# Performance work log

Hardware: AMD Instinct MI355X
Metric: run time of the kernel (lower is better)

Reference implementation:

```python
import jax, jax.numpy as jnp
import numpy as np

N_NODES = 10000
N_EDGES = 320000
D = 128  # feature dim for edges, nodes, globals


def setup_inputs() -> dict:
    key = jax.random.key(0)
    ks = jax.random.split(key, 8)
    edges = jax.random.normal(ks[0], (N_EDGES, D), dtype=jnp.float32)
    nodes = jax.random.normal(ks[1], (N_NODES, D), dtype=jnp.float32)
    globals_ = jax.random.normal(ks[2], (D,), dtype=jnp.float32)
    receivers = jax.random.randint(ks[3], (N_EDGES,), 0, N_NODES, dtype=jnp.int32).astype(jnp.int64)
    senders = jax.random.randint(ks[4], (N_EDGES,), 0, N_NODES, dtype=jnp.int32).astype(jnp.int64)
    W1 = jax.random.normal(ks[5], (4 * D, 256), dtype=jnp.float32) * (1.0 / np.sqrt(4 * D))
    b1 = jnp.zeros((256,), dtype=jnp.float32)
    W2 = jax.random.normal(ks[6], (256, D), dtype=jnp.float32) * (1.0 / np.sqrt(256))
    b2 = jnp.zeros((D,), dtype=jnp.float32)
    return {"edges": edges, "nodes": nodes, "globals_": globals_,
            "receivers": receivers, "senders": senders,
            "W1": W1, "b1": b1, "W2": W2, "b2": b2}


def reference(edges, nodes, globals_, receivers, senders, W1, b1, W2, b2):
    # Gather adjacent node features to edges, broadcast globals, concat.
    recv_feats = nodes[receivers]                 # [E, D]
    send_feats = nodes[senders]                   # [E, D]
    glob_feats = jnp.broadcast_to(globals_, (edges.shape[0], globals_.shape[0]))  # [E, D]
    x = jnp.concatenate([edges, recv_feats, send_feats, glob_feats], axis=-1)     # [E, 4D]
    # Edge-update MLP: 4D -> 256 -> D with relu.
    h = jax.nn.relu(x @ W1 + b1)
    new_edges = h @ W2 + b2                       # [E, D]
    return new_edges
```

## Files before the change

### kernel.cpp

```cpp
#include <hip/hip_runtime.h>
#include <hip/hip_bf16.h>

#define D 128
#define NH 256
#define K1 384
#define BM 64
#define E_TOTAL 320000
#define NNODES 10000

typedef __attribute__((ext_vector_type(8))) short bf16x8;
typedef __attribute__((ext_vector_type(4))) float f32x4;

__device__ __forceinline__ unsigned short f2b(float f) {
  unsigned int u = __builtin_bit_cast(unsigned int, f);
  u += 0x7fffu + ((u >> 16) & 1u);
  return (unsigned short)(u >> 16);
}

__global__ void cast_nodes_kernel(const float* __restrict__ nodes,
                                  ushort* __restrict__ out) {
  int i = (blockIdx.x * 256 + threadIdx.x) * 4;
  float4 v = *(const float4*)(nodes + i);
  ushort4 b;
  b.x = f2b(v.x); b.y = f2b(v.y); b.z = f2b(v.z); b.w = f2b(v.w);
  *(ushort4*)(out + i) = b;
}

__global__ void pack_w1_kernel(const float* __restrict__ W1,
                               ushort* __restrict__ W1p) {
  int c = blockIdx.x * 256 + threadIdx.x;
  int nt = c / (12 * 64);
  int rem = c % (12 * 64);
  int ks = rem >> 6;
  int l = rem & 63;
  int col = nt * 16 + (l & 15);
  int k0 = ks * 32 + (l >> 4) * 8;
  ushort* dst = W1p + (size_t)c * 8;
  #pragma unroll
  for (int j = 0; j < 8; ++j)
    dst[j] = f2b(W1[(size_t)(k0 + j) * NH + col]);
}

__global__ void pack_w2_kernel(const float* __restrict__ W2,
                               ushort* __restrict__ W2p) {
  int c = blockIdx.x * 256 + threadIdx.x;
  int nt2 = c / (8 * 64);
  int rem = c % (8 * 64);
  int ks = rem >> 6;
  int l = rem & 63;
  int col = nt2 * 16 + (l & 15);
  int k0 = ks * 32 + (l >> 4) * 8;
  ushort* dst = W2p + (size_t)c * 8;
  #pragma unroll
  for (int j = 0; j < 8; ++j)
    dst[j] = f2b(W2[(size_t)(k0 + j) * D + col]);
}

__global__ void cvec_kernel(const float* __restrict__ W1,
                            const float* __restrict__ b1,
                            const float* __restrict__ g,
                            float* __restrict__ cvec) {
  int n = threadIdx.x;
  float acc = b1[n];
  for (int k = 0; k < D; ++k)
    acc += g[k] * W1[(size_t)(K1 + k) * NH + n];
  cvec[n] = acc;
}

__global__ __launch_bounds__(512, 4) void fused_kernel(
    const float* __restrict__ edges,
    const ushort* __restrict__ nodes_b,
    const int* __restrict__ receivers,
    const int* __restrict__ senders,
    const ushort* __restrict__ W1p,
    const float* __restrict__ cvec,
    const ushort* __restrict__ W2p,
    const float* __restrict__ b2,
    float* __restrict__ out) {
  __shared__ char Xs[BM * 768];
  __shared__ char Hs[BM * 512];

  const int ebase = blockIdx.x * BM;
  const int tid = threadIdx.x;

  const int gr0 = tid >> 4;
  const int gr1 = gr0 + 32;
  const int gc = (tid & 15) << 3;
  int idx_r0 = receivers[ebase + gr0];
  int idx_r1 = receivers[ebase + gr1];
  int idx_s0 = senders[ebase + gr0];
  int idx_s1 = senders[ebase + gr1];

  float4 ev[4];
  int er[4], ec[4];
  #pragma unroll
  for (int it = 0; it < 4; ++it) {
    int ch = tid + it * 512;
    er[it] = ch >> 5;
    ec[it] = (ch & 31) << 2;
    ev[it] = *(const float4*)(edges + (size_t)(ebase + er[it]) * D + ec[it]);
  }

  uint4 gv[4];
  gv[0] = *(const uint4*)(nodes_b + (size_t)idx_r0 * D + gc);
  gv[1] = *(const uint4*)(nodes_b + (size_t)idx_r1 * D + gc);
  gv[2] = *(const uint4*)(nodes_b + (size_t)idx_s0 * D + gc);
  gv[3] = *(const uint4*)(nodes_b + (size_t)idx_s1 * D + gc);

  #pragma unroll
  for (int it = 0; it < 4; ++it) {
    ushort4 b;
    b.x = f2b(ev[it].x); b.y = f2b(ev[it].y); b.z = f2b(ev[it].z); b.w = f2b(ev[it].w);
    *(ushort4*)(Xs + er[it] * 768 + ((ec[it] * 2) ^ ((er[it] & 7) << 4))) = b;
  }
  {
    int cR = (D + gc) * 2, cS = (2 * D + gc) * 2;
    *(uint4*)(Xs + gr0 * 768 + (cR ^ ((gr0 & 7) << 4))) = gv[0];
    *(uint4*)(Xs + gr1 * 768 + (cR ^ ((gr1 & 7) << 4))) = gv[1];
    *(uint4*)(Xs + gr0 * 768 + (cS ^ ((gr0 & 7) << 4))) = gv[2];
    *(uint4*)(Xs + gr1 * 768 + (cS ^ ((gr1 & 7) << 4))) = gv[3];
  }
  __syncthreads();

  const int lane = tid & 63;
  const int wave = tid >> 6;
  const int lr = lane & 15;
  const int kg = lane >> 4;
  const int wm = wave >> 2;
  const int wn = wave & 3;

  float cv[4];
  #pragma unroll
  for (int n = 0; n < 4; ++n) cv[n] = cvec[wn * 64 + n * 16 + lr];
  float bias2[2];
  #pragma unroll
  for (int n = 0; n < 2; ++n) bias2[n] = b2[wn * 32 + n * 16 + lr];

  const ushort* w1base = W1p + (size_t)(wn * 4) * 12 * 512 + lane * 8;

  f32x4 acc[2][4] = {};
  bf16x8 bb[2][4];
  #pragma unroll
  for (int n = 0; n < 4; ++n)
    bb[0][n] = *(const bf16x8*)(w1base + (size_t)n * 12 * 512);

  #pragma unroll
  for (int ks = 0; ks < 12; ++ks) {
    const int cur = ks & 1, nxt = cur ^ 1;
    if (ks < 11) {
      #pragma unroll
      for (int n = 0; n < 4; ++n)
        bb[nxt][n] = *(const bf16x8*)(w1base + (size_t)n * 12 * 512 + (ks + 1) * 512);
    }
    const int k0 = ks * 32 + kg * 8;
    bf16x8 a[2];
    #pragma unroll
    for (int m = 0; m < 2; ++m) {
      int row = wm * 32 + m * 16 + lr;
      a[m] = *(const bf16x8*)(Xs + row * 768 + ((k0 * 2) ^ ((row & 7) << 4)));
    }
    #pragma unroll
    for (int m = 0; m < 2; ++m)
      #pragma unroll
      for (int n = 0; n < 4; ++n)
        acc[m][n] = __builtin_amdgcn_mfma_f32_16x16x32_bf16(a[m], bb[cur][n], acc[m][n], 0, 0, 0);
  }

  #pragma unroll
  for (int n = 0; n < 4; ++n) {
    int col = wn * 64 + n * 16 + lr;
    #pragma unroll
    for (int m = 0; m < 2; ++m) {
      #pragma unroll
      for (int r = 0; r < 4; ++r) {
        int row = wm * 32 + m * 16 + kg * 4 + r;
        float v = acc[m][n][r] + cv[n];
        v = v > 0.f ? v : 0.f;
        *(ushort*)(Hs + row * 512 + ((col * 2) ^ ((row & 7) << 4))) = f2b(v);
      }
    }
  }

  const ushort* w2base = W2p + (size_t)(wn * 2) * 8 * 512 + lane * 8;
  bf16x8 b2b[2][2];
  #pragma unroll
  for (int n = 0; n < 2; ++n)
    b2b[0][n] = *(const bf16x8*)(w2base + (size_t)n * 8 * 512);
  __syncthreads();

  f32x4 acc2[2][2] = {};
  #pragma unroll
  for (int ks = 0; ks < 8; ++ks) {
    const int cur = ks & 1, nxt = cur ^ 1;
    if (ks < 7) {
      #pragma unroll
      for (int n = 0; n < 2; ++n)
        b2b[nxt][n] = *(const bf16x8*)(w2base + (size_t)n * 8 * 512 + (ks + 1) * 512);
    }
    const int k0 = ks * 32 + kg * 8;
    bf16x8 a[2];
    #pragma unroll
    for (int m = 0; m < 2; ++m) {
      int row = wm * 32 + m * 16 + lr;
      a[m] = *(const bf16x8*)(Hs + row * 512 + ((k0 * 2) ^ ((row & 7) << 4)));
    }
    #pragma unroll
    for (int m = 0; m < 2; ++m)
      #pragma unroll
      for (int n = 0; n < 2; ++n)
        acc2[m][n] = __builtin_amdgcn_mfma_f32_16x16x32_bf16(a[m], b2b[cur][n], acc2[m][n], 0, 0, 0);
  }

  #pragma unroll
  for (int n = 0; n < 2; ++n) {
    int col = wn * 32 + n * 16 + lr;
    #pragma unroll
    for (int m = 0; m < 2; ++m) {
      #pragma unroll
      for (int r = 0; r < 4; ++r) {
        int row = wm * 32 + m * 16 + kg * 4 + r;
        out[(size_t)(ebase + row) * D + col] = acc2[m][n][r] + bias2[n];
      }
    }
  }
}

extern "C" void kernel_launch(void* const* d_in, const int* in_sizes, int n_in,
                              void* d_out, int out_size, void* d_ws, size_t ws_size,
                              hipStream_t stream) {
  const float* edges     = (const float*)d_in[0];
  const float* nodes     = (const float*)d_in[1];
  const float* globals_  = (const float*)d_in[2];
  const int*   receivers = (const int*)d_in[3];
  const int*   senders   = (const int*)d_in[4];
  const float* W1        = (const float*)d_in[5];
  const float* b1        = (const float*)d_in[6];
  const float* W2        = (const float*)d_in[7];
  const float* b2        = (const float*)d_in[8];
  float* out = (float*)d_out;

  char* ws = (char*)d_ws;
  ushort* nodes_b = (ushort*)ws;
  ushort* W1p     = (ushort*)(ws + 2560000);
  ushort* W2p     = (ushort*)(ws + 2560000 + 196608);
  float*  cvec    = (float*)(ws + 2560000 + 196608 + 65536);

  hipLaunchKernelGGL(cast_nodes_kernel, dim3(NNODES * D / 1024), dim3(256), 0, stream,
                     nodes, nodes_b);
  hipLaunchKernelGGL(pack_w1_kernel, dim3(48), dim3(256), 0, stream, W1, W1p);
  hipLaunchKernelGGL(pack_w2_kernel, dim3(16), dim3(256), 0, stream, W2, W2p);
  hipLaunchKernelGGL(cvec_kernel, dim3(1), dim3(256), 0, stream,
                     W1, b1, globals_, cvec);
  hipLaunchKernelGGL(fused_kernel, dim3(E_TOTAL / BM), dim3(512), 0, stream,
                     edges, nodes_b, receivers, senders, W1p, cvec, W2p, b2, out);
}
```

Baseline: 160.7 us.

## Use 4 waves per block with full-M wave tiles and alias H into X LDS

The block shrinks from 512 to 256 threads. Each wave now covers all 64 rows and a wider column slice, so every weight fragment loaded from global memory feeds four MFMAs instead of two, halving redundant W1/W2 fetches per block. The hidden buffer now reuses the X shared memory, with an extra barrier before H is written, which cuts LDS per block so more blocks can be resident. The cost is more accumulator registers per thread and less latency hiding inside each block.

After: 153.2 us. -4.7%, faster.

```diff
diff --git a/kernel.cpp b/kernel.cpp
--- a/kernel.cpp
+++ b/kernel.cpp
@@ -67,7 +67,7 @@
   cvec[n] = acc;
 }
 
-__global__ __launch_bounds__(512, 4) void fused_kernel(
+__global__ __launch_bounds__(256, 3) void fused_kernel(
     const float* __restrict__ edges,
     const ushort* __restrict__ nodes_b,
     const int* __restrict__ receivers,
@@ -78,47 +78,52 @@
     const float* __restrict__ b2,
     float* __restrict__ out) {
   __shared__ char Xs[BM * 768];
-  __shared__ char Hs[BM * 512];
+  char* Hs = Xs;
 
   const int ebase = blockIdx.x * BM;
   const int tid = threadIdx.x;
 
-  const int gr0 = tid >> 4;
-  const int gr1 = gr0 + 32;
+  const int rb = tid >> 4;
   const int gc = (tid & 15) << 3;
-  int idx_r0 = receivers[ebase + gr0];
-  int idx_r1 = receivers[ebase + gr1];
-  int idx_s0 = senders[ebase + gr0];
-  int idx_s1 = senders[ebase + gr1];
-
-  float4 ev[4];
-  int er[4], ec[4];
-  #pragma unroll
-  for (int it = 0; it < 4; ++it) {
-    int ch = tid + it * 512;
-    er[it] = ch >> 5;
-    ec[it] = (ch & 31) << 2;
-    ev[it] = *(const float4*)(edges + (size_t)(ebase + er[it]) * D + ec[it]);
-  }
-
-  uint4 gv[4];
-  gv[0] = *(const uint4*)(nodes_b + (size_t)idx_r0 * D + gc);
-  gv[1] = *(const uint4*)(nodes_b + (size_t)idx_r1 * D + gc);
-  gv[2] = *(const uint4*)(nodes_b + (size_t)idx_s0 * D + gc);
-  gv[3] = *(const uint4*)(nodes_b + (size_t)idx_s1 * D + gc);
-
-  #pragma unroll
-  for (int it = 0; it < 4; ++it) {
+  int idxR[4], idxS[4];
+  #pragma unroll
+  for (int j = 0; j < 4; ++j) {
+    idxR[j] = receivers[ebase + rb + j * 16];
+    idxS[j] = senders[ebase + rb + j * 16];
+  }
+
+  float4 ev[8];
+  #pragma unroll
+  for (int it = 0; it < 8; ++it) {
+    int c = tid + it * 256;
+    int row = c >> 5, colc = (c & 31) << 2;
+    ev[it] = *(const float4*)(edges + (size_t)(ebase + row) * D + colc);
+  }
+
+  uint4 gvR[4], gvS[4];
+  #pragma unroll
+  for (int j = 0; j < 4; ++j) {
+    gvR[j] = *(const uint4*)(nodes_b + (size_t)idxR[j] * D + gc);
+    gvS[j] = *(const uint4*)(nodes_b + (size_t)idxS[j] * D + gc);
+  }
+
+  #pragma unroll
+  for (int it = 0; it < 8; ++it) {
+    int c = tid + it * 256;
+    int row = c >> 5, colc = (c & 31) << 2;
     ushort4 b;
     b.x = f2b(ev[it].x); b.y = f2b(ev[it].y); b.z = f2b(ev[it].z); b.w = f2b(ev[it].w);
-    *(ushort4*)(Xs + er[it] * 768 + ((ec[it] * 2) ^ ((er[it] & 7) << 4))) = b;
+    *(ushort4*)(Xs + row * 768 + ((colc * 2) ^ ((row & 7) << 4))) = b;
   }
   {
-    int cR = (D + gc) * 2, cS = (2 * D + gc) * 2;
-    *(uint4*)(Xs + gr0 * 768 + (cR ^ ((gr0 & 7) << 4))) = gv[0];
-    *(uint4*)(Xs + gr1 * 768 + (cR ^ ((gr1 & 7) << 4))) = gv[1];
-    *(uint4*)(Xs + gr0 * 768 + (cS ^ ((gr0 & 7) << 4))) = gv[2];
-    *(uint4*)(Xs + gr1 * 768 + (cS ^ ((gr1 & 7) << 4))) = gv[3];
+    const int cR = (D + gc) * 2, cS = (2 * D + gc) * 2;
+    #pragma unroll
+    for (int j = 0; j < 4; ++j) {
+      int row = rb + j * 16;
+      int sw = (row & 7) << 4;
+      *(uint4*)(Xs + row * 768 + (cR ^ sw)) = gvR[j];
+      *(uint4*)(Xs + row * 768 + (cS ^ sw)) = gvS[j];
+    }
   }
   __syncthreads();
 
@@ -126,19 +131,17 @@
   const int wave = tid >> 6;
   const int lr = lane & 15;
   const int kg = lane >> 4;
-  const int wm = wave >> 2;
-  const int wn = wave & 3;
 
   float cv[4];
   #pragma unroll
-  for (int n = 0; n < 4; ++n) cv[n] = cvec[wn * 64 + n * 16 + lr];
+  for (int n = 0; n < 4; ++n) cv[n] = cvec[wave * 64 + n * 16 + lr];
   float bias2[2];
   #pragma unroll
-  for (int n = 0; n < 2; ++n) bias2[n] = b2[wn * 32 + n * 16 + lr];
-
-  const ushort* w1base = W1p + (size_t)(wn * 4) * 12 * 512 + lane * 8;
-
-  f32x4 acc[2][4] = {};
+  for (int n = 0; n < 2; ++n) bias2[n] = b2[wave * 32 + n * 16 + lr];
+
+  const ushort* w1base = W1p + (size_t)(wave * 4) * 12 * 512 + lane * 8;
+
+  f32x4 acc[4][4] = {};
   bf16x8 bb[2][4];
   #pragma unroll
   for (int n = 0; n < 4; ++n)
@@ -153,42 +156,44 @@
         bb[nxt][n] = *(const bf16x8*)(w1base + (size_t)n * 12 * 512 + (ks + 1) * 512);
     }
     const int k0 = ks * 32 + kg * 8;
-    bf16x8 a[2];
-    #pragma unroll
-    for (int m = 0; m < 2; ++m) {
-      int row = wm * 32 + m * 16 + lr;
+    bf16x8 a[4];
+    #pragma unroll
+    for (int m = 0; m < 4; ++m) {
+      int row = m * 16 + lr;
       a[m] = *(const bf16x8*)(Xs + row * 768 + ((k0 * 2) ^ ((row & 7) << 4)));
     }
     #pragma unroll
-    for (int m = 0; m < 2; ++m)
+    for (int m = 0; m < 4; ++m)
       #pragma unroll
       for (int n = 0; n < 4; ++n)
         acc[m][n] = __builtin_amdgcn_mfma_f32_16x16x32_bf16(a[m], bb[cur][n], acc[m][n], 0, 0, 0);
   }
 
+  const ushort* w2base = W2p + (size_t)(wave * 2) * 8 * 512 + lane * 8;
+  bf16x8 b2b[2][2];
+  #pragma unroll
+  for (int n = 0; n < 2; ++n)
+    b2b[0][n] = *(const bf16x8*)(w2base + (size_t)n * 8 * 512);
+
+  __syncthreads();
+
   #pragma unroll
   for (int n = 0; n < 4; ++n) {
-    int col = wn * 64 + n * 16 + lr;
-    #pragma unroll
-    for (int m = 0; m < 2; ++m) {
+    int col = wave * 64 + n * 16 + lr;
+    #pragma unroll
+    for (int m = 0; m < 4; ++m) {
       #pragma unroll
       for (int r = 0; r < 4; ++r) {
-        int row = wm * 32 + m * 16 + kg * 4 + r;
+        int row = m * 16 + kg * 4 + r;
         float v = acc[m][n][r] + cv[n];
         v = v > 0.f ? v : 0.f;
         *(ushort*)(Hs + row * 512 + ((col * 2) ^ ((row & 7) << 4))) = f2b(v);
       }
     }
   }
-
-  const ushort* w2base = W2p + (size_t)(wn * 2) * 8 * 512 + lane * 8;
-  bf16x8 b2b[2][2];
-  #pragma unroll
-  for (int n = 0; n < 2; ++n)
-    b2b[0][n] = *(const bf16x8*)(w2base + (size_t)n * 8 * 512);
   __syncthreads();
 
-  f32x4 acc2[2][2] = {};
+  f32x4 acc2[4][2] = {};
   #pragma unroll
   for (int ks = 0; ks < 8; ++ks) {
     const int cur = ks & 1, nxt = cur ^ 1;
@@ -198,14 +203,14 @@
         b2b[nxt][n] = *(const bf16x8*)(w2base + (size_t)n * 8 * 512 + (ks + 1) * 512);
     }
     const int k0 = ks * 32 + kg * 8;
-    bf16x8 a[2];
-    #pragma unroll
-    for (int m = 0; m < 2; ++m) {
-      int row = wm * 32 + m * 16 + lr;
+    bf16x8 a[4];
+    #pragma unroll
+    for (int m = 0; m < 4; ++m) {
+      int row = m * 16 + lr;
       a[m] = *(const bf16x8*)(Hs + row * 512 + ((k0 * 2) ^ ((row & 7) << 4)));
     }
     #pragma unroll
-    for (int m = 0; m < 2; ++m)
+    for (int m = 0; m < 4; ++m)
       #pragma unroll
       for (int n = 0; n < 2; ++n)
         acc2[m][n] = __builtin_amdgcn_mfma_f32_16x16x32_bf16(a[m], b2b[cur][n], acc2[m][n], 0, 0, 0);
@@ -213,12 +218,12 @@
 
   #pragma unroll
   for (int n = 0; n < 2; ++n) {
-    int col = wn * 32 + n * 16 + lr;
-    #pragma unroll
-    for (int m = 0; m < 2; ++m) {
+    int col = wave * 32 + n * 16 + lr;
+    #pragma unroll
+    for (int m = 0; m < 4; ++m) {
       #pragma unroll
       for (int r = 0; r < 4; ++r) {
-        int row = wm * 32 + m * 16 + kg * 4 + r;
+        int row = m * 16 + kg * 4 + r;
         out[(size_t)(ebase + row) * D + col] = acc2[m][n][r] + bias2[n];
       }
     }
@@ -251,6 +256,6 @@
   hipLaunchKernelGGL(pack_w2_kernel, dim3(16), dim3(256), 0, stream, W2, W2p);
   hipLaunchKernelGGL(cvec_kernel, dim3(1), dim3(256), 0, stream,
                      W1, b1, globals_, cvec);
-  hipLaunchKernelGGL(fused_kernel, dim3(E_TOTAL / BM), dim3(512), 0, stream,
+  hipLaunchKernelGGL(fused_kernel, dim3(E_TOTAL / BM), dim3(256), 0, stream,
                      edges, nodes_b, receivers, senders, W1p, cvec, W2p, b2, out);
 }
```
